# Performance work log

Hardware: AMD Instinct MI355X
Metric: run time of the kernel (lower is better)

The kernel has to match this reference:

```python
import jax, jax.numpy as jnp
import numpy as np


def fwht(x):
    """Unnormalized Fast Walsh-Hadamard transform along axis 0 (Sylvester order).
    Equivalent to H @ x where H is the +/-1 Hadamard matrix. x.shape[0] must be a power of 2."""
    D = x.shape[0]
    orig_shape = x.shape
    x = x.reshape(D, -1)
    h = 1
    while h < D:
        x = x.reshape(D // (2 * h), 2, h, -1)
        a = x[:, 0]
        b = x[:, 1]
        x = jnp.stack([a + b, a - b], axis=1)
        h *= 2
    return x.reshape(orig_shape)


def setup_inputs() -> dict:
    D = 4096
    B = 2048
    key = jax.random.key(0)
    k_x, k_eps, k_rho = jax.random.split(key, 3)
    x = jax.random.normal(k_x, (B, D), dtype=jnp.float32)
    epsilon = jax.random.normal(k_eps, (D,), dtype=jnp.float32)
    s1 = jnp.ones((D,), dtype=jnp.float32) * 0.01
    s2 = jnp.ones((D,), dtype=jnp.float32) * 0.01
    g_mu = jnp.zeros((D,), dtype=jnp.float32)
    # g_rho ~ Uniform(-5, -4) as in the torch init
    g_rho = jax.random.uniform(k_rho, (D,), dtype=jnp.float32, minval=-5.0, maxval=-4.0)
    return {"x": x, "epsilon": epsilon, "s1": s1, "s2": s2, "g_mu": g_mu, "g_rho": g_rho}


def reference(x, epsilon, s1, s2, g_mu, g_rho):
    D = s1.shape[0]
    # g_sigma_sqrt_diagonal = softplus(g_rho); sampled diag g = g_mu + sigma * eps.
    # W = diag(s1) @ H @ diag(g) @ H @ diag(s2); mu and sigma terms are linear in g, so combine.
    g = g_mu + jax.nn.softplus(g_rho) * epsilon
    # HS2 = H * s2 (columns of H scaled by s2) = H @ diag(s2) = fwht(diag(s2)) along axis 0
    HS2 = fwht(jnp.diag(s2))                      # [D, D]
    W = s1[:, None] * fwht(g[:, None] * HS2)      # [D, D]
    # F.linear(x, W) = x @ W^T
    return x @ W.T
```

## Files before the change

kernel.cpp:

```cpp
#include <hip/hip_runtime.h>
#include <math.h>

#define DIM 4096
#define ROWS 2048
#define SB 68

typedef _Float16 half8  __attribute__((ext_vector_type(8)));
typedef _Float16 half4  __attribute__((ext_vector_type(4)));
typedef float    float4e __attribute__((ext_vector_type(4)));

__global__ void g_precompute(const float* __restrict__ eps,
                             const float* __restrict__ g_mu,
                             const float* __restrict__ g_rho,
                             float* __restrict__ g) {
    int i = blockIdx.x * blockDim.x + threadIdx.x;
    g[i] = fmaf(log1pf(expf(g_rho[i])), eps[i], g_mu[i]);
}

__device__ __forceinline__ void hx_stage(const _Float16* __restrict__ img,
                                         int n, int q, const half8 Hf[4][2],
                                         float4e acc[4][4]) {
    half8 B[4][2];
#pragma unroll
    for (int J = 0; J < 4; ++J)
#pragma unroll
        for (int Kt = 0; Kt < 2; ++Kt) {
            const _Float16* p = img + (32 * Kt + 8 * q) * SB + 16 * J + n;
            half8 b;
#pragma unroll
            for (int j = 0; j < 8; ++j) b[j] = p[j * SB];
            B[J][Kt] = b;
        }
#pragma unroll
    for (int I = 0; I < 4; ++I)
#pragma unroll
        for (int J = 0; J < 4; ++J) {
            float4e c = {0.0f, 0.0f, 0.0f, 0.0f};
            c = __builtin_amdgcn_mfma_f32_16x16x32_f16(Hf[I][0], B[J][0], c, 0, 0, 0);
            c = __builtin_amdgcn_mfma_f32_16x16x32_f16(Hf[I][1], B[J][1], c, 0, 0, 0);
            acc[I][J] = c;
        }
}

__device__ __forceinline__ void img_write_T(_Float16* __restrict__ img,
                                            int n, int q, const float4e acc[4][4]) {
#pragma unroll
    for (int I = 0; I < 4; ++I)
#pragma unroll
        for (int J = 0; J < 4; ++J) {
            half4 h;
            h[0] = (_Float16)acc[I][J][0];
            h[1] = (_Float16)acc[I][J][1];
            h[2] = (_Float16)acc[I][J][2];
            h[3] = (_Float16)acc[I][J][3];
            *(half4*)(img + (16 * J + n) * SB + 16 * I + 4 * q) = h;
        }
}

__global__ void __launch_bounds__(256, 2)
whvi_mfma(const float* __restrict__ x, const float* __restrict__ s1,
          const float* __restrict__ s2, const float* __restrict__ g,
          float* __restrict__ out) {
    const int lane = threadIdx.x & 63;
    const int wid  = threadIdx.x >> 6;
    const int row  = blockIdx.x * 4 + wid;
    const int n = lane & 15, q = lane >> 4;

    __shared__ __align__(16) _Float16 lds[4 * 64 * SB];
    _Float16* __restrict__ img = lds + wid * 64 * SB;

    const float4e* __restrict__ xr  = (const float4e*)(x + (size_t)row * DIM);
    const float4e* __restrict__ s2v = (const float4e*)s2;

    float4e xv[16], sv[16];
#pragma unroll
    for (int r = 0; r < 16; ++r) xv[r] = xr[64 * r + lane];
#pragma unroll
    for (int r = 0; r < 16; ++r) sv[r] = s2v[64 * r + lane];

    half8 Hf[4][2];
#pragma unroll
    for (int I = 0; I < 4; ++I)
#pragma unroll
        for (int Kt = 0; Kt < 2; ++Kt) {
            half8 h;
#pragma unroll
            for (int j = 0; j < 8; ++j) {
                int rr = 16 * I + n, cc = 32 * Kt + 8 * q + j;
                h[j] = (__popc(rr & cc) & 1) ? (_Float16)(-1.0f) : (_Float16)(1.0f);
            }
            Hf[I][Kt] = h;
        }

#pragma unroll
    for (int r = 0; r < 16; ++r) {
        float4e p = xv[r] * sv[r];
        half4 h;
        h[0] = (_Float16)p[0]; h[1] = (_Float16)p[1];
        h[2] = (_Float16)p[2]; h[3] = (_Float16)p[3];
        *(half4*)(img + (4 * r + q) * SB + 4 * n) = h;
    }

    float4e acc[4][4];

    hx_stage(img, n, q, Hf, acc);
    img_write_T(img, n, q, acc);
    hx_stage(img, n, q, Hf, acc);

#pragma unroll
    for (int I = 0; I < 4; ++I)
#pragma unroll
        for (int J = 0; J < 4; ++J) {
            const float4e gg = *(const float4e*)(g + 1024 * J + 64 * n + 16 * I + 4 * q);
            acc[I][J] *= gg;
        }

    img_write_T(img, n, q, acc);
    hx_stage(img, n, q, Hf, acc);
    img_write_T(img, n, q, acc);
    hx_stage(img, n, q, Hf, acc);

    float* __restrict__ orow = out + (size_t)row * DIM;
#pragma unroll
    for (int I = 0; I < 4; ++I)
#pragma unroll
        for (int J = 0; J < 4; ++J) {
            const int e = 1024 * J + 64 * n + 16 * I + 4 * q;
            const float4e sg = *(const float4e*)(s1 + e);
            *(float4e*)(orow + e) = acc[I][J] * sg;
        }
}

extern "C" void kernel_launch(void* const* d_in, const int* in_sizes, int n_in,
                              void* d_out, int out_size, void* d_ws, size_t ws_size,
                              hipStream_t stream) {
    const float* x     = (const float*)d_in[0];
    const float* eps   = (const float*)d_in[1];
    const float* s1    = (const float*)d_in[2];
    const float* s2    = (const float*)d_in[3];
    const float* g_mu  = (const float*)d_in[4];
    const float* g_rho = (const float*)d_in[5];
    float* out = (float*)d_out;
    float* g   = (float*)d_ws;

    g_precompute<<<DIM / 256, 256, 0, stream>>>(eps, g_mu, g_rho, g);
    whvi_mfma<<<ROWS / 4, 256, 0, stream>>>(x, s1, s2, g, out);
}
```

Before: 100.8 us.

## Use vectorized LDS fragment loads by alternating left/right Hadamard multiplies

Replaces the strided 8-element scalar LDS gathers with single half8 vector loads by reading fragments along rows. To keep the math consistent, it alternates multiplying by H on the right and on the left, which changes how the 64x64 image is oriented between stages. The g vector is stored transposed in the precompute kernel to match the new orientation, and the LDS row stride goes from 68 to 72 halves so rows stay 16-byte aligned for vector reads. The added padding uses a little more LDS and may change the bank-conflict pattern.

```diff
diff --git a/kernel.cpp b/kernel.cpp
--- a/kernel.cpp
+++ b/kernel.cpp
@@ -3,7 +3,7 @@
 
 #define DIM 4096
 #define ROWS 2048
-#define SB 68
+#define SB 72
 
 typedef _Float16 half8  __attribute__((ext_vector_type(8)));
 typedef _Float16 half4  __attribute__((ext_vector_type(4)));
@@ -12,32 +12,42 @@
 __global__ void g_precompute(const float* __restrict__ eps,
                              const float* __restrict__ g_mu,
                              const float* __restrict__ g_rho,
-                             float* __restrict__ g) {
+                             float* __restrict__ gt) {
     int i = blockIdx.x * blockDim.x + threadIdx.x;
-    g[i] = fmaf(log1pf(expf(g_rho[i])), eps[i], g_mu[i]);
+    gt[((i & 63) << 6) | (i >> 6)] = fmaf(log1pf(expf(g_rho[i])), eps[i], g_mu[i]);
 }
 
-__device__ __forceinline__ void hx_stage(const _Float16* __restrict__ img,
-                                         int n, int q, const half8 Hf[4][2],
-                                         float4e acc[4][4]) {
-    half8 B[4][2];
+__device__ __forceinline__ void load_frags(const _Float16* __restrict__ img,
+                                           int n, int q, half8 frag[4][2]) {
 #pragma unroll
-    for (int J = 0; J < 4; ++J)
+    for (int F = 0; F < 4; ++F)
 #pragma unroll
-        for (int Kt = 0; Kt < 2; ++Kt) {
-            const _Float16* p = img + (32 * Kt + 8 * q) * SB + 16 * J + n;
-            half8 b;
-#pragma unroll
-            for (int j = 0; j < 8; ++j) b[j] = p[j * SB];
-            B[J][Kt] = b;
-        }
+        for (int Kt = 0; Kt < 2; ++Kt)
+            frag[F][Kt] = *(const half8*)(img + (16 * F + n) * SB + 32 * Kt + 8 * q);
+}
+
+__device__ __forceinline__ void mul_H_right(const half8 frag[4][2], const half8 Hf[4][2],
+                                            float4e acc[4][4]) {
 #pragma unroll
     for (int I = 0; I < 4; ++I)
 #pragma unroll
         for (int J = 0; J < 4; ++J) {
             float4e c = {0.0f, 0.0f, 0.0f, 0.0f};
-            c = __builtin_amdgcn_mfma_f32_16x16x32_f16(Hf[I][0], B[J][0], c, 0, 0, 0);
-            c = __builtin_amdgcn_mfma_f32_16x16x32_f16(Hf[I][1], B[J][1], c, 0, 0, 0);
+            c = __builtin_amdgcn_mfma_f32_16x16x32_f16(frag[I][0], Hf[J][0], c, 0, 0, 0);
+            c = __builtin_amdgcn_mfma_f32_16x16x32_f16(frag[I][1], Hf[J][1], c, 0, 0, 0);
+            acc[I][J] = c;
+        }
+}
+
+__device__ __forceinline__ void mul_H_left(const half8 frag[4][2], const half8 Hf[4][2],
+                                           float4e acc[4][4]) {
+#pragma unroll
+    for (int I = 0; I < 4; ++I)
+#pragma unroll
+        for (int J = 0; J < 4; ++J) {
+            float4e c = {0.0f, 0.0f, 0.0f, 0.0f};
+            c = __builtin_amdgcn_mfma_f32_16x16x32_f16(Hf[I][0], frag[J][0], c, 0, 0, 0);
+            c = __builtin_amdgcn_mfma_f32_16x16x32_f16(Hf[I][1], frag[J][1], c, 0, 0, 0);
             acc[I][J] = c;
         }
 }
@@ -59,7 +69,7 @@
 
 __global__ void __launch_bounds__(256, 2)
 whvi_mfma(const float* __restrict__ x, const float* __restrict__ s1,
-          const float* __restrict__ s2, const float* __restrict__ g,
+          const float* __restrict__ s2, const float* __restrict__ gt,
           float* __restrict__ out) {
     const int lane = threadIdx.x & 63;
     const int wid  = threadIdx.x >> 6;
@@ -101,24 +111,30 @@
         *(half4*)(img + (4 * r + q) * SB + 4 * n) = h;
     }
 
+    half8   frag[4][2];
     float4e acc[4][4];
 
-    hx_stage(img, n, q, Hf, acc);
+    load_frags(img, n, q, frag);
+    mul_H_right(frag, Hf, acc);
     img_write_T(img, n, q, acc);
-    hx_stage(img, n, q, Hf, acc);
+
+    load_frags(img, n, q, frag);
+    mul_H_left(frag, Hf, acc);
 
 #pragma unroll
     for (int I = 0; I < 4; ++I)
 #pragma unroll
         for (int J = 0; J < 4; ++J) {
-            const float4e gg = *(const float4e*)(g + 1024 * J + 64 * n + 16 * I + 4 * q);
+            const float4e gg = *(const float4e*)(gt + 1024 * J + 64 * n + 16 * I + 4 * q);
             acc[I][J] *= gg;
         }
 
     img_write_T(img, n, q, acc);
-    hx_stage(img, n, q, Hf, acc);
+    load_frags(img, n, q, frag);
+    mul_H_right(frag, Hf, acc);
     img_write_T(img, n, q, acc);
-    hx_stage(img, n, q, Hf, acc);
+    load_frags(img, n, q, frag);
+    mul_H_left(frag, Hf, acc);
 
     float* __restrict__ orow = out + (size_t)row * DIM;
 #pragma unroll
@@ -141,8 +157,8 @@
     const float* g_mu  = (const float*)d_in[4];
     const float* g_rho = (const float*)d_in[5];
     float* out = (float*)d_out;
-    float* g   = (float*)d_ws;
+    float* gt  = (float*)d_ws;
 
-    g_precompute<<<DIM / 256, 256, 0, stream>>>(eps, g_mu, g_rho, g);
-    whvi_mfma<<<ROWS / 4, 256, 0, stream>>>(x, s1, s2, g, out);
+    g_precompute<<<DIM / 256, 256, 0, stream>>>(eps, g_mu, g_rho, gt);
+    whvi_mfma<<<ROWS / 4, 256, 0, stream>>>(x, s1, s2, gt, out);
 }
```

Result: no change. 100.1 us, median of 2 (-0.7%).
